# Optimization experiments

Measured on AMD Instinct MI355X. Metric: run time of the kernel, lower is better.

Reference implementation:

```python
import jax, jax.numpy as jnp
import numpy as np

B, S, E = 2, 2048, 1024
H, D = 16, 64  # num_heads, head_dim


def setup_inputs() -> dict:
    key = jax.random.key(0)
    k1, k2, k3 = jax.random.split(key, 3)
    x = jax.random.normal(k1, (B, S, E), dtype=jnp.float32)
    # nnx normal() init has stddev 0.01; scale to keep magnitudes realistic
    w_qkv = jax.random.normal(k2, (E, H, 3 * D), dtype=jnp.float32) * 0.01
    w_out = jax.random.normal(k3, (H, D, E), dtype=jnp.float32) * 0.01
    return {"x": x, "w_qkv": w_qkv, "w_out": w_out}


def _attention(q, k, v):
    # q,k,v: [B, S, H, D]
    dtype = q.dtype
    logits = jnp.einsum('bqhd,bkhd->bhqk', q.astype(jnp.float32), k.astype(jnp.float32))
    logits = logits / jnp.sqrt(jnp.float32(q.shape[-1]))
    mask = jnp.tril(jnp.ones((q.shape[1], q.shape[1]), dtype=jnp.bool_))
    neg = jnp.asarray(-0.7 * jnp.finfo(logits.dtype).max, dtype=logits.dtype)
    logits = jnp.where(mask, logits, neg)
    probs = jax.nn.softmax(logits, axis=-1).astype(dtype)
    return jnp.einsum('bhqk,bkhd->bqhd', probs, v)


def reference(x, w_qkv, w_out):
    # qkv projection: [B,S,E] x [E,H,3D] -> [B,S,H,3D]
    qkv = jnp.einsum('bse,ehd->bshd', x, w_qkv)
    q, k, v = jnp.split(qkv, 3, axis=-1)
    out = _attention(q, k, v)  # [B,S,H,D]
    # output projection contracts (H,D) -> E
    return jnp.einsum('bshd,hde->bse', out, w_out)
```

## Files before the change

kernel.cpp:

```cpp
#include <hip/hip_runtime.h>

typedef unsigned short u16;
typedef unsigned int u32;
typedef __attribute__((ext_vector_type(8))) short bf16x8;
typedef __attribute__((ext_vector_type(4))) float f32x4;
typedef __attribute__((ext_vector_type(16))) float f32x16;
typedef __attribute__((ext_vector_type(4))) u32 u32x4;

#define MFMA16(a, b, c) __builtin_amdgcn_mfma_f32_16x16x32_bf16((a), (b), (c), 0, 0, 0)
#define MFMA32(a, b, c) __builtin_amdgcn_mfma_f32_32x32x16_bf16((a), (b), (c), 0, 0, 0)

__device__ __forceinline__ void async_lds16(void* lds, const void* g) {
  __builtin_amdgcn_global_load_lds(
      (const __attribute__((address_space(1))) void*)g,
      (__attribute__((address_space(3))) void*)lds, 16, 0, 0);
}

__device__ __forceinline__ u16 f2bf(float f) {
  union { float f; unsigned u; } v; v.f = f;
  unsigned r = v.u + 0x7fffu + ((v.u >> 16) & 1u);
  return (u16)(r >> 16);
}

__device__ __forceinline__ u32 cvt_pk_bf16(float lo, float hi) {
  u32 r;
  asm("v_cvt_pk_bf16_f32 %0, %1, %2" : "=v"(r) : "v"(lo), "v"(hi));
  return r;
}

__device__ __forceinline__ float exp2_fast(float x) {
  float r;
  asm("v_exp_f32 %0, %1" : "=v"(r) : "v"(x));
  return r;
}

__device__ __forceinline__ void pswap(u32& a, u32& b) {
  asm("v_permlane32_swap_b32 %0, %1" : "+v"(a), "+v"(b));
}


__device__ __forceinline__ void transpose_cvt_body(const float* __restrict__ in, u16* __restrict__ out,
                                                   int R, int C, int bx, int by,
                                                   float (*tile)[33]) {
  int c0 = bx * 32, r0 = by * 32;
  int tx = threadIdx.x & 31, ty = threadIdx.x >> 5;
#pragma unroll
  for (int i = 0; i < 32; i += 8)
    tile[ty + i][tx] = in[(long)(r0 + ty + i) * C + c0 + tx];
  __syncthreads();
#pragma unroll
  for (int i = 0; i < 32; i += 8)
    out[(long)(c0 + ty + i) * R + r0 + tx] = f2bf(tile[tx][ty + i]);
}

__global__ __launch_bounds__(256) void k_prep(const float* __restrict__ x, u16* __restrict__ xb,
                                              const float* __restrict__ w_qkv, u16* __restrict__ wqkvT,
                                              const float* __restrict__ w_out, u16* __restrict__ woutT) {
  __shared__ float tile[32][33];
  const int B = blockIdx.x;
  if (B < 4096) {
    int i = (B * 256 + threadIdx.x) * 4;
    float4 v = *(const float4*)(x + i);
    ushort4 o;
    o.x = f2bf(v.x); o.y = f2bf(v.y); o.z = f2bf(v.z); o.w = f2bf(v.w);
    *(ushort4*)(xb + i) = o;
  } else if (B < 7168) {
    int bb = B - 4096;
    transpose_cvt_body(w_qkv, wqkvT, 1024, 3072, bb % 96, bb / 96, tile);
  } else {
    int bb = B - 7168;
    transpose_cvt_body(w_out, woutT, 1024, 1024, bb & 31, bb >> 5, tile);
  }
}


template <int BM, int BN, int NW, int WN, int WCS, int MR, int NR, int NLD>
__device__ __forceinline__ void gemm_core_pipe(const u16* __restrict__ A, const u16* __restrict__ Bt,
                                               int K, long row0, long col0,
                                               u16* sA, u16* sB, f32x4 (&acc)[MR][NR]) {
  const int NTHR = NW * 64;
  const int ABYTES = BM * 64 * 2;
  const int BBYTES = BN * 64 * 2;
  const int t = threadIdx.x;
  const int lane = t & 63, g = lane >> 4, m16 = lane & 15;
  const int wid = t >> 6, wr = wid / WN, wc = wid % WN;
  const int nkt = K >> 6;

  auto stage = [&](int buf, int kt) {
    const int k0 = kt << 6;
#pragma unroll
    for (int it = 0; it < ABYTES / (NTHR * 16); ++it) {
      int i = it * NTHR + t;
      int r = i >> 3, c = i & 7, cs = c ^ (r & 7);
      async_lds16((char*)sA + buf * ABYTES + i * 16, A + (row0 + r) * K + k0 + cs * 8);
    }
#pragma unroll
    for (int it = 0; it < BBYTES / (NTHR * 16); ++it) {
      int i = it * NTHR + t;
      int r = i >> 3, c = i & 7, cs = c ^ (r & 7);
      async_lds16((char*)sB + buf * BBYTES + i * 16, Bt + (col0 + r) * K + k0 + cs * 8);
    }
  };

  stage(0, 0);
  stage(1, 1);
  int cur = 0;
  for (int kt = 0; kt < nkt; ++kt) {
    if (kt + 1 < nkt) {
      if constexpr (NLD == 7) asm volatile("s_waitcnt vmcnt(7)" ::: "memory");
      else                    asm volatile("s_waitcnt vmcnt(8)" ::: "memory");
    } else {
      asm volatile("s_waitcnt vmcnt(0)" ::: "memory");
    }
    __builtin_amdgcn_s_barrier();
    __builtin_amdgcn_sched_barrier(0);
    const char* bA = (const char*)sA + cur * ABYTES;
    const char* bB = (const char*)sB + cur * BBYTES;
#pragma unroll
    for (int kk6 = 0; kk6 < 2; ++kk6) {
      const int ke = kk6 * 32 + 8 * g;
      bf16x8 av[MR], bv[NR];
#pragma unroll
      for (int mi = 0; mi < MR; ++mi) {
        int row = wr * (MR * 16) + mi * 16 + m16;
        av[mi] = *(const bf16x8*)(bA + (row << 7) + ((ke << 1) ^ ((row & 7) << 4)));
      }
#pragma unroll
      for (int ni = 0; ni < NR; ++ni) {
        int row = wc * WCS + ni * 16 + m16;
        bv[ni] = *(const bf16x8*)(bB + (row << 7) + ((ke << 1) ^ ((row & 7) << 4)));
      }
#pragma unroll
      for (int mi = 0; mi < MR; ++mi)
#pragma unroll
        for (int ni = 0; ni < NR; ++ni)
          acc[mi][ni] = MFMA16(av[mi], bv[ni], acc[mi][ni]);
    }
    __builtin_amdgcn_sched_barrier(0);
    __builtin_amdgcn_s_barrier();
    if (kt + 2 < nkt) stage(cur, kt + 2);
    cur ^= 1;
  }
}

__global__ __launch_bounds__(512, 2) void k_gemm_qkv(const u16* __restrict__ xb, const u16* __restrict__ wT,
                                                     u16* __restrict__ Qo, u16* __restrict__ Ko,
                                                     u16* __restrict__ Vt) {
  __shared__ __align__(16) u16 sA[2 * 256 * 64];
  __shared__ __align__(16) u16 sB[2 * 192 * 64];
  f32x4 acc[8][3];
  const f32x4 z = {0.f, 0.f, 0.f, 0.f};
#pragma unroll
  for (int mi = 0; mi < 8; ++mi)
#pragma unroll
    for (int ni = 0; ni < 3; ++ni) acc[mi][ni] = z;
  const int L = blockIdx.x;
  const int xcd = L & 7, idx = L >> 3;
  const int rowt = xcd * 2 + (idx & 1);
  const int colt = idx >> 1;
  long row0 = (long)rowt * 256, col0 = (long)colt * 192;
  gemm_core_pipe<256, 192, 8, 4, 48, 8, 3, 7>(xb, wT, 1024, row0, col0, sA, sB, acc);
  const int t = threadIdx.x;
  const int lane = t & 63, g = lane >> 4, m16 = lane & 15;
  const int wid = t >> 6, wr = wid >> 2, wc = wid & 3;
  const int h = colt;
#pragma unroll
  for (int mi = 0; mi < 8; ++mi) {
#pragma unroll
    for (int ni = 0; ni < 3; ++ni) {
      int rem = wc * 48 + ni * 16 + m16;
      int which = rem >> 6, d = rem & 63;
      int row_base = (int)row0 + wr * 128 + mi * 16 + 4 * g;
      int b = row_base >> 11, s = row_base & 2047;
      if (which == 2) {
        ushort4 o;
        o.x = f2bf(acc[mi][ni][0]); o.y = f2bf(acc[mi][ni][1]);
        o.z = f2bf(acc[mi][ni][2]); o.w = f2bf(acc[mi][ni][3]);
        *(ushort4*)(Vt + ((long)(b * 16 + h)) * 131072 + (long)d * 2048 + s) = o;
      } else {
        long off = (((long)(b * 16 + h)) * 2048 + s) * 64 + d;
#pragma unroll
        for (int r = 0; r < 4; ++r) {
          float v = acc[mi][ni][r];
          if (which == 0) Qo[off + (long)r * 64] = f2bf(v * 0.18033688f);
          else            Ko[off + (long)r * 64] = f2bf(v);
        }
      }
    }
  }
}

__global__ __launch_bounds__(256) void k_gemm_out(const u16* __restrict__ Ob, const u16* __restrict__ wT,
                                                  float* __restrict__ out) {
  __shared__ __align__(16) u16 sA[2 * 128 * 64];
  __shared__ __align__(16) u16 sB[2 * 128 * 64];
  f32x4 acc[4][4];
  const f32x4 z = {0.f, 0.f, 0.f, 0.f};
#pragma unroll
  for (int mi = 0; mi < 4; ++mi)
#pragma unroll
    for (int ni = 0; ni < 4; ++ni) acc[mi][ni] = z;
  const int L = blockIdx.x;
  const int xcd = L & 7, idx = L >> 3;
  const int rowt = xcd * 4 + (idx & 3);
  const int colt = idx >> 2;
  long row0 = (long)rowt * 128, col0 = (long)colt * 128;
  gemm_core_pipe<128, 128, 4, 2, 64, 4, 4, 8>(Ob, wT, 1024, row0, col0, sA, sB, acc);
  const int t = threadIdx.x;
  const int lane = t & 63, g = lane >> 4, m16 = lane & 15;
  const int wid = t >> 6, wr = wid >> 1, wc = wid & 1;
#pragma unroll
  for (int mi = 0; mi < 4; ++mi) {
#pragma unroll
    for (int ni = 0; ni < 4; ++ni) {
#pragma unroll
      for (int r = 0; r < 4; ++r) {
        long row = row0 + wr * 64 + mi * 16 + 4 * g + r;
        long col = col0 + wc * 64 + ni * 16 + m16;
        out[row * 1024 + col] = acc[mi][ni][r];
      }
    }
  }
}


template <bool DIAG>
__device__ __forceinline__ void attn_sub(const char* Kt, const char* Vt, int bsub,
                                         bf16x8 qf0, bf16x8 qf1, bf16x8 qf2, bf16x8 qf3,
                                         f32x16& acc0, f32x16& acc1, float& l,
                                         int q5, int hi) {
  const int x7 = q5 & 7;
  const int rowK = (bsub * 32 + q5) << 7;
  bf16x8 k0 = *(const bf16x8*)(Kt + rowK + (((0 + hi) ^ x7) << 4));
  bf16x8 k1 = *(const bf16x8*)(Kt + rowK + (((2 + hi) ^ x7) << 4));
  bf16x8 k2 = *(const bf16x8*)(Kt + rowK + (((4 + hi) ^ x7) << 4));
  bf16x8 k3 = *(const bf16x8*)(Kt + rowK + (((6 + hi) ^ x7) << 4));
  const int rowV0 = q5 << 7, rowV1 = (q5 + 32) << 7;
  bf16x8 v00 = *(const bf16x8*)(Vt + rowV0 + (((bsub * 4 + 0 + hi) ^ x7) << 4));
  bf16x8 v01 = *(const bf16x8*)(Vt + rowV1 + (((bsub * 4 + 0 + hi) ^ x7) << 4));
  bf16x8 v10 = *(const bf16x8*)(Vt + rowV0 + (((bsub * 4 + 2 + hi) ^ x7) << 4));
  bf16x8 v11 = *(const bf16x8*)(Vt + rowV1 + (((bsub * 4 + 2 + hi) ^ x7) << 4));

  f32x16 s;
#pragma unroll
  for (int r = 0; r < 16; ++r) s[r] = 0.f;
  __builtin_amdgcn_s_setprio(1);
  s = MFMA32(k0, qf0, s);
  s = MFMA32(k1, qf1, s);
  s = MFMA32(k2, qf2, s);
  s = MFMA32(k3, qf3, s);
  __builtin_amdgcn_s_setprio(0);

  float p[16];
#pragma unroll
  for (int r = 0; r < 16; ++r) {
    float pv = exp2_fast(s[r]);
    if (DIAG) {
      int crow = (r & 3) + 8 * (r >> 2) + 4 * hi;
      pv = (crow <= q5) ? pv : 0.f;
    }
    p[r] = pv;
  }
  l += (((p[0] + p[1]) + (p[2] + p[3])) + ((p[4] + p[5]) + (p[6] + p[7]))) +
       (((p[8] + p[9]) + (p[10] + p[11])) + ((p[12] + p[13]) + (p[14] + p[15])));

  u32 a0 = cvt_pk_bf16(p[0], p[1]), a1 = cvt_pk_bf16(p[2], p[3]);
  u32 b0 = cvt_pk_bf16(p[4], p[5]), b1 = cvt_pk_bf16(p[6], p[7]);
  pswap(a0, b0); pswap(a1, b1);
  u32 c0 = cvt_pk_bf16(p[8], p[9]), c1 = cvt_pk_bf16(p[10], p[11]);
  u32 d0 = cvt_pk_bf16(p[12], p[13]), d1 = cvt_pk_bf16(p[14], p[15]);
  pswap(c0, d0); pswap(c1, d1);
  u32x4 t0; t0[0] = a0; t0[1] = a1; t0[2] = b0; t0[3] = b1;
  u32x4 t1; t1[0] = c0; t1[1] = c1; t1[2] = d0; t1[3] = d1;
  bf16x8 pa0 = __builtin_bit_cast(bf16x8, t0);
  bf16x8 pa1 = __builtin_bit_cast(bf16x8, t1);

  __builtin_amdgcn_s_setprio(1);
  acc0 = MFMA32(pa0, v00, acc0);
  acc1 = MFMA32(pa0, v01, acc1);
  acc0 = MFMA32(pa1, v10, acc0);
  acc1 = MFMA32(pa1, v11, acc1);
  __builtin_amdgcn_s_setprio(0);
}

__global__ __launch_bounds__(256) void k_attn(const u16* __restrict__ Qg, const u16* __restrict__ Kg,
                                              const u16* __restrict__ Vtg, u16* __restrict__ Og) {
  __shared__ __align__(16) u16 sK[4][64 * 64];
  __shared__ __align__(16) u16 sV[4][64 * 64];
  const int t = threadIdx.x;
  const int lane = t & 63, q5 = lane & 31, hi = lane >> 5, w = t >> 6;
  const int L = blockIdx.x;
  const int bh = L & 31, pr = L >> 5;
  const int qtA = pr, qtB = 15 - pr;
  const int b = bh >> 4, h = bh & 15;
  const u16* Qh = Qg + (long)bh * 131072;
  const u16* Kh = Kg + (long)bh * 131072;
  const u16* Vh = Vtg + (long)bh * 131072;
  char* sKb = (char*)sK;
  char* sVb = (char*)sV;

  const int sL_ = qtA * 4 + w, sH_ = qtB * 4 + w;
  const int q0L = sL_ * 32, q0H = sH_ * 32;
  const int nkt = 2 * qtB + 2;

  const u16* QpL = Qh + (long)(q0L + q5) * 64 + hi * 8;
  bf16x8 qfL0 = *(const bf16x8*)(QpL);
  bf16x8 qfL1 = *(const bf16x8*)(QpL + 16);
  bf16x8 qfL2 = *(const bf16x8*)(QpL + 32);
  bf16x8 qfL3 = *(const bf16x8*)(QpL + 48);
  const u16* QpH = Qh + (long)(q0H + q5) * 64 + hi * 8;
  bf16x8 qfH0 = *(const bf16x8*)(QpH);
  bf16x8 qfH1 = *(const bf16x8*)(QpH + 16);
  bf16x8 qfH2 = *(const bf16x8*)(QpH + 32);
  bf16x8 qfH3 = *(const bf16x8*)(QpH + 48);

  f32x16 aL0, aL1, aH0, aH1;
#pragma unroll
  for (int r = 0; r < 16; ++r) { aL0[r] = 0.f; aL1[r] = 0.f; aH0[r] = 0.f; aH1[r] = 0.f; }
  float lL = 0.f, lH = 0.f;

  auto stage = [&](int buf, int kt) {
    const int kbase = kt << 6;
#pragma unroll
    for (int ps = 0; ps < 2; ++ps) {
      int i = ps * 256 + t;
      int r = i >> 3, c = i & 7, cs = c ^ (r & 7);
      async_lds16(sKb + buf * 8192 + i * 16, Kh + (long)(kbase + r) * 64 + cs * 8);
    }
#pragma unroll
    for (int ps = 0; ps < 2; ++ps) {
      int i = ps * 256 + t;
      int d = i >> 3, c = i & 7, cs = c ^ (d & 7);
      async_lds16(sVb + buf * 8192 + i * 16, Vh + (long)d * 2048 + kbase + cs * 8);
    }
  };

  stage(0, 0);
  stage(1, 1);
  stage(2, 2);
#pragma unroll 1
  for (int kt = 0; kt < nkt; ++kt) {
    const int rem = nkt - kt;
    if (rem >= 3)      asm volatile("s_waitcnt vmcnt(8)" ::: "memory");
    else if (rem == 2) asm volatile("s_waitcnt vmcnt(4)" ::: "memory");
    else               asm volatile("s_waitcnt vmcnt(0)" ::: "memory");
    __builtin_amdgcn_s_barrier();
    __builtin_amdgcn_sched_barrier(0);
    if (kt + 3 < nkt) stage((kt + 3) & 3, kt + 3);
    const char* Kt = sKb + (kt & 3) * 8192;
    const char* Vt = sVb + (kt & 3) * 8192;
    const int c2 = 2 * kt;
    if (c2 <= sH_) {
      if (c2 == sH_) attn_sub<true>(Kt, Vt, 0, qfH0, qfH1, qfH2, qfH3, aH0, aH1, lH, q5, hi);
      else           attn_sub<false>(Kt, Vt, 0, qfH0, qfH1, qfH2, qfH3, aH0, aH1, lH, q5, hi);
    }
    if (c2 + 1 <= sH_) {
      if (c2 + 1 == sH_) attn_sub<true>(Kt, Vt, 1, qfH0, qfH1, qfH2, qfH3, aH0, aH1, lH, q5, hi);
      else               attn_sub<false>(Kt, Vt, 1, qfH0, qfH1, qfH2, qfH3, aH0, aH1, lH, q5, hi);
    }
    if (c2 <= sL_) {
      if (c2 == sL_) attn_sub<true>(Kt, Vt, 0, qfL0, qfL1, qfL2, qfL3, aL0, aL1, lL, q5, hi);
      else           attn_sub<false>(Kt, Vt, 0, qfL0, qfL1, qfL2, qfL3, aL0, aL1, lL, q5, hi);
    }
    if (c2 + 1 <= sL_) {
      if (c2 + 1 == sL_) attn_sub<true>(Kt, Vt, 1, qfL0, qfL1, qfL2, qfL3, aL0, aL1, lL, q5, hi);
      else               attn_sub<false>(Kt, Vt, 1, qfL0, qfL1, qfL2, qfL3, aL0, aL1, lL, q5, hi);
    }
  }

  const long orow_base = (long)b * 2048;
  lH += __shfl_xor(lH, 32);
  float liH = 1.0f / lH;
#pragma unroll
  for (int r = 0; r < 16; ++r) {
    int crow = (r & 3) + 8 * (r >> 2) + 4 * hi;
    float lf = __shfl(liH, crow);
    long orow = orow_base + q0H + crow;
    Og[orow * 1024 + h * 64 + q5] = f2bf(aH0[r] * lf);
    Og[orow * 1024 + h * 64 + 32 + q5] = f2bf(aH1[r] * lf);
  }
  lL += __shfl_xor(lL, 32);
  float liL = 1.0f / lL;
#pragma unroll
  for (int r = 0; r < 16; ++r) {
    int crow = (r & 3) + 8 * (r >> 2) + 4 * hi;
    float lf = __shfl(liL, crow);
    long orow = orow_base + q0L + crow;
    Og[orow * 1024 + h * 64 + q5] = f2bf(aL0[r] * lf);
    Og[orow * 1024 + h * 64 + 32 + q5] = f2bf(aL1[r] * lf);
  }
}


extern "C" void kernel_launch(void* const* d_in, const int* in_sizes, int n_in,
                              void* d_out, int out_size, void* d_ws, size_t ws_size,
                              hipStream_t stream) {
  const float* x = (const float*)d_in[0];
  const float* w_qkv = (const float*)d_in[1];
  const float* w_out = (const float*)d_in[2];
  float* out = (float*)d_out;
  char* ws = (char*)d_ws;

  u16* xb    = (u16*)(ws + 0);
  u16* wqkvT = (u16*)(ws + 8388608L);
  u16* woutT = (u16*)(ws + 14680064L);
  u16* Qb    = (u16*)(ws + 16777216L);
  u16* Kb    = (u16*)(ws + 25165824L);
  u16* Vt    = (u16*)(ws + 33554432L);
  u16* Ob    = xb;

  k_prep<<<dim3(8192), 256, 0, stream>>>(x, xb, w_qkv, wqkvT, w_out, woutT);
  k_gemm_qkv<<<dim3(256), 512, 0, stream>>>(xb, wqkvT, Qb, Kb, Vt);
  k_attn<<<dim3(256), 256, 0, stream>>>(Qb, Kb, Vt, Ob);
  k_gemm_out<<<dim3(256), 256, 0, stream>>>(Ob, woutT, out);
}
```

Baseline: 113.4 us.

## Use 128-key tiles with double buffering in attention kernel

Doubles the K/V tile from 64 to 128 keys per stage and switches from a 4-deep ring of 64-key buffers to two 128-key buffers. This halves loop iterations and barriers per block. A second barrier is added after compute so the next stage can reuse the buffer safely. The trade-off is less prefetch depth, an extra barrier per iteration, and coarser causal granularity (more skipped-branch checks per tile).

```diff
diff --git a/kernel.cpp b/kernel.cpp
--- a/kernel.cpp
+++ b/kernel.cpp
@@ -235,7 +235,7 @@
   bf16x8 k1 = *(const bf16x8*)(Kt + rowK + (((2 + hi) ^ x7) << 4));
   bf16x8 k2 = *(const bf16x8*)(Kt + rowK + (((4 + hi) ^ x7) << 4));
   bf16x8 k3 = *(const bf16x8*)(Kt + rowK + (((6 + hi) ^ x7) << 4));
-  const int rowV0 = q5 << 7, rowV1 = (q5 + 32) << 7;
+  const int rowV0 = q5 << 8, rowV1 = (q5 + 32) << 8;
   bf16x8 v00 = *(const bf16x8*)(Vt + rowV0 + (((bsub * 4 + 0 + hi) ^ x7) << 4));
   bf16x8 v01 = *(const bf16x8*)(Vt + rowV1 + (((bsub * 4 + 0 + hi) ^ x7) << 4));
   bf16x8 v10 = *(const bf16x8*)(Vt + rowV0 + (((bsub * 4 + 2 + hi) ^ x7) << 4));
@@ -285,8 +285,8 @@
 
 __global__ __launch_bounds__(256) void k_attn(const u16* __restrict__ Qg, const u16* __restrict__ Kg,
                                               const u16* __restrict__ Vtg, u16* __restrict__ Og) {
-  __shared__ __align__(16) u16 sK[4][64 * 64];
-  __shared__ __align__(16) u16 sV[4][64 * 64];
+  __shared__ __align__(16) u16 sK[2][128 * 64];
+  __shared__ __align__(16) u16 sV[2][64 * 128];
   const int t = threadIdx.x;
   const int lane = t & 63, q5 = lane & 31, hi = lane >> 5, w = t >> 6;
   const int L = blockIdx.x;
@@ -301,7 +301,7 @@
 
   const int sL_ = qtA * 4 + w, sH_ = qtB * 4 + w;
   const int q0L = sL_ * 32, q0H = sH_ * 32;
-  const int nkt = 2 * qtB + 2;
+  const int nkt = qtB + 1;
 
   const u16* QpL = Qh + (long)(q0L + q5) * 64 + hi * 8;
   bf16x8 qfL0 = *(const bf16x8*)(QpL);
@@ -320,52 +320,67 @@
   float lL = 0.f, lH = 0.f;
 
   auto stage = [&](int buf, int kt) {
-    const int kbase = kt << 6;
-#pragma unroll
-    for (int ps = 0; ps < 2; ++ps) {
+    const int kbase = kt << 7;
+#pragma unroll
+    for (int ps = 0; ps < 4; ++ps) {
       int i = ps * 256 + t;
       int r = i >> 3, c = i & 7, cs = c ^ (r & 7);
-      async_lds16(sKb + buf * 8192 + i * 16, Kh + (long)(kbase + r) * 64 + cs * 8);
-    }
-#pragma unroll
-    for (int ps = 0; ps < 2; ++ps) {
+      async_lds16(sKb + buf * 16384 + i * 16, Kh + (long)(kbase + r) * 64 + cs * 8);
+    }
+#pragma unroll
+    for (int ps = 0; ps < 4; ++ps) {
       int i = ps * 256 + t;
-      int d = i >> 3, c = i & 7, cs = c ^ (d & 7);
-      async_lds16(sVb + buf * 8192 + i * 16, Vh + (long)d * 2048 + kbase + cs * 8);
+      int d = i >> 4, c = i & 15, cs = c ^ (d & 7);
+      async_lds16(sVb + buf * 16384 + i * 16, Vh + (long)d * 2048 + kbase + cs * 8);
     }
   };
 
   stage(0, 0);
   stage(1, 1);
-  stage(2, 2);
 #pragma unroll 1
   for (int kt = 0; kt < nkt; ++kt) {
-    const int rem = nkt - kt;
-    if (rem >= 3)      asm volatile("s_waitcnt vmcnt(8)" ::: "memory");
-    else if (rem == 2) asm volatile("s_waitcnt vmcnt(4)" ::: "memory");
-    else               asm volatile("s_waitcnt vmcnt(0)" ::: "memory");
+    if (kt + 1 < nkt) asm volatile("s_waitcnt vmcnt(8)" ::: "memory");
+    else              asm volatile("s_waitcnt vmcnt(0)" ::: "memory");
     __builtin_amdgcn_s_barrier();
     __builtin_amdgcn_sched_barrier(0);
-    if (kt + 3 < nkt) stage((kt + 3) & 3, kt + 3);
-    const char* Kt = sKb + (kt & 3) * 8192;
-    const char* Vt = sVb + (kt & 3) * 8192;
-    const int c2 = 2 * kt;
-    if (c2 <= sH_) {
-      if (c2 == sH_) attn_sub<true>(Kt, Vt, 0, qfH0, qfH1, qfH2, qfH3, aH0, aH1, lH, q5, hi);
+    const char* Kt = sKb + (kt & 1) * 16384;
+    const char* Vt = sVb + (kt & 1) * 16384;
+    const int c4 = 4 * kt;
+    if (c4 <= sH_) {
+      if (c4 == sH_) attn_sub<true>(Kt, Vt, 0, qfH0, qfH1, qfH2, qfH3, aH0, aH1, lH, q5, hi);
       else           attn_sub<false>(Kt, Vt, 0, qfH0, qfH1, qfH2, qfH3, aH0, aH1, lH, q5, hi);
     }
-    if (c2 + 1 <= sH_) {
-      if (c2 + 1 == sH_) attn_sub<true>(Kt, Vt, 1, qfH0, qfH1, qfH2, qfH3, aH0, aH1, lH, q5, hi);
+    if (c4 + 1 <= sH_) {
+      if (c4 + 1 == sH_) attn_sub<true>(Kt, Vt, 1, qfH0, qfH1, qfH2, qfH3, aH0, aH1, lH, q5, hi);
       else               attn_sub<false>(Kt, Vt, 1, qfH0, qfH1, qfH2, qfH3, aH0, aH1, lH, q5, hi);
     }
-    if (c2 <= sL_) {
-      if (c2 == sL_) attn_sub<true>(Kt, Vt, 0, qfL0, qfL1, qfL2, qfL3, aL0, aL1, lL, q5, hi);
+    if (c4 + 2 <= sH_) {
+      if (c4 + 2 == sH_) attn_sub<true>(Kt, Vt, 2, qfH0, qfH1, qfH2, qfH3, aH0, aH1, lH, q5, hi);
+      else               attn_sub<false>(Kt, Vt, 2, qfH0, qfH1, qfH2, qfH3, aH0, aH1, lH, q5, hi);
+    }
+    if (c4 + 3 <= sH_) {
+      if (c4 + 3 == sH_) attn_sub<true>(Kt, Vt, 3, qfH0, qfH1, qfH2, qfH3, aH0, aH1, lH, q5, hi);
+      else               attn_sub<false>(Kt, Vt, 3, qfH0, qfH1, qfH2, qfH3, aH0, aH1, lH, q5, hi);
+    }
+    if (c4 <= sL_) {
+      if (c4 == sL_) attn_sub<true>(Kt, Vt, 0, qfL0, qfL1, qfL2, qfL3, aL0, aL1, lL, q5, hi);
       else           attn_sub<false>(Kt, Vt, 0, qfL0, qfL1, qfL2, qfL3, aL0, aL1, lL, q5, hi);
     }
-    if (c2 + 1 <= sL_) {
-      if (c2 + 1 == sL_) attn_sub<true>(Kt, Vt, 1, qfL0, qfL1, qfL2, qfL3, aL0, aL1, lL, q5, hi);
+    if (c4 + 1 <= sL_) {
+      if (c4 + 1 == sL_) attn_sub<true>(Kt, Vt, 1, qfL0, qfL1, qfL2, qfL3, aL0, aL1, lL, q5, hi);
       else               attn_sub<false>(Kt, Vt, 1, qfL0, qfL1, qfL2, qfL3, aL0, aL1, lL, q5, hi);
     }
+    if (c4 + 2 <= sL_) {
+      if (c4 + 2 == sL_) attn_sub<true>(Kt, Vt, 2, qfL0, qfL1, qfL2, qfL3, aL0, aL1, lL, q5, hi);
+      else               attn_sub<false>(Kt, Vt, 2, qfL0, qfL1, qfL2, qfL3, aL0, aL1, lL, q5, hi);
+    }
+    if (c4 + 3 <= sL_) {
+      if (c4 + 3 == sL_) attn_sub<true>(Kt, Vt, 3, qfL0, qfL1, qfL2, qfL3, aL0, aL1, lL, q5, hi);
+      else               attn_sub<false>(Kt, Vt, 3, qfL0, qfL1, qfL2, qfL3, aL0, aL1, lL, q5, hi);
+    }
+    __builtin_amdgcn_sched_barrier(0);
+    __builtin_amdgcn_s_barrier();
+    if (kt + 2 < nkt) stage(kt & 1, kt + 2);
   }
 
   const long orow_base = (long)b * 2048;
```

Measured after the change: 103.0 us, median of 2. 1.1x faster.

## Enlarge attention KV tiles to 256 keys with double-buffered LDS staging

Applied to the files above, without the earlier changes.

Each key/value tile staged into LDS now holds 256 keys instead of 64, using two buffers instead of four. This cuts the number of loop iterations, barriers and waitcnt points per block, and each iteration now runs up to eight 32-key sub-blocks back to back. In exchange the block uses 128KB of LDS, and the next tile is prefetched only after compute finishes, behind a second barrier. That prefetch has less distance ahead of its use, and the causal tail may load keys that are never used.

```diff
diff --git a/kernel.cpp b/kernel.cpp
--- a/kernel.cpp
+++ b/kernel.cpp
@@ -235,7 +235,7 @@
   bf16x8 k1 = *(const bf16x8*)(Kt + rowK + (((2 + hi) ^ x7) << 4));
   bf16x8 k2 = *(const bf16x8*)(Kt + rowK + (((4 + hi) ^ x7) << 4));
   bf16x8 k3 = *(const bf16x8*)(Kt + rowK + (((6 + hi) ^ x7) << 4));
-  const int rowV0 = q5 << 7, rowV1 = (q5 + 32) << 7;
+  const int rowV0 = q5 << 9, rowV1 = (q5 + 32) << 9;
   bf16x8 v00 = *(const bf16x8*)(Vt + rowV0 + (((bsub * 4 + 0 + hi) ^ x7) << 4));
   bf16x8 v01 = *(const bf16x8*)(Vt + rowV1 + (((bsub * 4 + 0 + hi) ^ x7) << 4));
   bf16x8 v10 = *(const bf16x8*)(Vt + rowV0 + (((bsub * 4 + 2 + hi) ^ x7) << 4));
@@ -285,8 +285,8 @@
 
 __global__ __launch_bounds__(256) void k_attn(const u16* __restrict__ Qg, const u16* __restrict__ Kg,
                                               const u16* __restrict__ Vtg, u16* __restrict__ Og) {
-  __shared__ __align__(16) u16 sK[4][64 * 64];
-  __shared__ __align__(16) u16 sV[4][64 * 64];
+  __shared__ __align__(16) u16 sK[2][256 * 64];
+  __shared__ __align__(16) u16 sV[2][64 * 256];
   const int t = threadIdx.x;
   const int lane = t & 63, q5 = lane & 31, hi = lane >> 5, w = t >> 6;
   const int L = blockIdx.x;
@@ -301,7 +301,7 @@
 
   const int sL_ = qtA * 4 + w, sH_ = qtB * 4 + w;
   const int q0L = sL_ * 32, q0H = sH_ * 32;
-  const int nkt = 2 * qtB + 2;
+  const int nkt = (qtB + 2) >> 1;
 
   const u16* QpL = Qh + (long)(q0L + q5) * 64 + hi * 8;
   bf16x8 qfL0 = *(const bf16x8*)(QpL);
@@ -320,52 +320,49 @@
   float lL = 0.f, lH = 0.f;
 
   auto stage = [&](int buf, int kt) {
-    const int kbase = kt << 6;
-#pragma unroll
-    for (int ps = 0; ps < 2; ++ps) {
+    const int kbase = kt << 8;
+#pragma unroll
+    for (int ps = 0; ps < 8; ++ps) {
       int i = ps * 256 + t;
       int r = i >> 3, c = i & 7, cs = c ^ (r & 7);
-      async_lds16(sKb + buf * 8192 + i * 16, Kh + (long)(kbase + r) * 64 + cs * 8);
-    }
-#pragma unroll
-    for (int ps = 0; ps < 2; ++ps) {
+      async_lds16(sKb + buf * 32768 + i * 16, Kh + (long)(kbase + r) * 64 + cs * 8);
+    }
+#pragma unroll
+    for (int ps = 0; ps < 8; ++ps) {
       int i = ps * 256 + t;
-      int d = i >> 3, c = i & 7, cs = c ^ (d & 7);
-      async_lds16(sVb + buf * 8192 + i * 16, Vh + (long)d * 2048 + kbase + cs * 8);
+      int d = i >> 5, c = i & 31, cs = c ^ (d & 7);
+      async_lds16(sVb + buf * 32768 + i * 16, Vh + (long)d * 2048 + kbase + cs * 8);
     }
   };
 
   stage(0, 0);
   stage(1, 1);
-  stage(2, 2);
 #pragma unroll 1
   for (int kt = 0; kt < nkt; ++kt) {
-    const int rem = nkt - kt;
-    if (rem >= 3)      asm volatile("s_waitcnt vmcnt(8)" ::: "memory");
-    else if (rem == 2) asm volatile("s_waitcnt vmcnt(4)" ::: "memory");
-    else               asm volatile("s_waitcnt vmcnt(0)" ::: "memory");
+    if (kt + 1 < nkt) asm volatile("s_waitcnt vmcnt(16)" ::: "memory");
+    else              asm volatile("s_waitcnt vmcnt(0)" ::: "memory");
     __builtin_amdgcn_s_barrier();
     __builtin_amdgcn_sched_barrier(0);
-    if (kt + 3 < nkt) stage((kt + 3) & 3, kt + 3);
-    const char* Kt = sKb + (kt & 3) * 8192;
-    const char* Vt = sVb + (kt & 3) * 8192;
-    const int c2 = 2 * kt;
-    if (c2 <= sH_) {
-      if (c2 == sH_) attn_sub<true>(Kt, Vt, 0, qfH0, qfH1, qfH2, qfH3, aH0, aH1, lH, q5, hi);
-      else           attn_sub<false>(Kt, Vt, 0, qfH0, qfH1, qfH2, qfH3, aH0, aH1, lH, q5, hi);
-    }
-    if (c2 + 1 <= sH_) {
-      if (c2 + 1 == sH_) attn_sub<true>(Kt, Vt, 1, qfH0, qfH1, qfH2, qfH3, aH0, aH1, lH, q5, hi);
-      else               attn_sub<false>(Kt, Vt, 1, qfH0, qfH1, qfH2, qfH3, aH0, aH1, lH, q5, hi);
-    }
-    if (c2 <= sL_) {
-      if (c2 == sL_) attn_sub<true>(Kt, Vt, 0, qfL0, qfL1, qfL2, qfL3, aL0, aL1, lL, q5, hi);
-      else           attn_sub<false>(Kt, Vt, 0, qfL0, qfL1, qfL2, qfL3, aL0, aL1, lL, q5, hi);
-    }
-    if (c2 + 1 <= sL_) {
-      if (c2 + 1 == sL_) attn_sub<true>(Kt, Vt, 1, qfL0, qfL1, qfL2, qfL3, aL0, aL1, lL, q5, hi);
-      else               attn_sub<false>(Kt, Vt, 1, qfL0, qfL1, qfL2, qfL3, aL0, aL1, lL, q5, hi);
-    }
+    const char* Kt = sKb + (kt & 1) * 32768;
+    const char* Vt = sVb + (kt & 1) * 32768;
+    const int c8 = 8 * kt;
+#pragma unroll
+    for (int j = 0; j < 8; ++j) {
+      if (c8 + j <= sH_) {
+        if (c8 + j == sH_) attn_sub<true>(Kt, Vt, j, qfH0, qfH1, qfH2, qfH3, aH0, aH1, lH, q5, hi);
+        else               attn_sub<false>(Kt, Vt, j, qfH0, qfH1, qfH2, qfH3, aH0, aH1, lH, q5, hi);
+      }
+    }
+#pragma unroll
+    for (int j = 0; j < 8; ++j) {
+      if (c8 + j <= sL_) {
+        if (c8 + j == sL_) attn_sub<true>(Kt, Vt, j, qfL0, qfL1, qfL2, qfL3, aL0, aL1, lL, q5, hi);
+        else               attn_sub<false>(Kt, Vt, j, qfL0, qfL1, qfL2, qfL3, aL0, aL1, lL, q5, hi);
+      }
+    }
+    __builtin_amdgcn_sched_barrier(0);
+    __builtin_amdgcn_s_barrier();
+    if (kt + 2 < nkt) stage(kt & 1, kt + 2);
   }
 
   const long orow_base = (long)b * 2048;
```

Measured after the change: 102.6 us. 9.5% less time.
